# Kernel tuning notes

Measured on AMD Instinct MI355X. Metric: run time of the kernel, lower is better.

Reference implementation:

```python
import jax, jax.numpy as jnp
import numpy as np

N, E, IN_DIM, HID, L = 50000, 800000, 64, 64, 3
EDGE_DIM = 2 * HID + 2  # src_h | dst_h | edge_feat


def setup_inputs() -> dict:
    key = jax.random.key(0)
    ks = jax.random.split(key, 32)
    s = 0.05
    inp = {
        "h": jax.random.normal(ks[0], (N, IN_DIM), jnp.float32),
        "e": jax.random.normal(ks[1], (E, 2), jnp.float32),
        "src": jax.random.randint(ks[2], (E,), 0, N),
        "dst": jax.random.randint(ks[3], (E,), 0, N),
        # input embedding
        "emb_W": jax.random.normal(ks[4], (IN_DIM, HID), jnp.float32) * s,
        "emb_b": jnp.zeros((HID,), jnp.float32),
        # per-GIN-layer params (stacked over L)
        "eps": jnp.zeros((L,), jnp.float32),  # learn_eps init 0
        "mlp_W1": jax.random.normal(ks[5], (L, HID, HID), jnp.float32) * s,
        "mlp_b1": jnp.zeros((L, HID), jnp.float32),
        "mlp_bn_s": jnp.ones((L, HID), jnp.float32),   # eval-mode BN folded: x*s+sh
        "mlp_bn_sh": jnp.zeros((L, HID), jnp.float32),
        "mlp_W2": jax.random.normal(ks[6], (L, HID, HID), jnp.float32) * s,
        "mlp_b2": jnp.zeros((L, HID), jnp.float32),
        "apply_bn_s": jnp.ones((L, HID), jnp.float32),
        "apply_bn_sh": jnp.zeros((L, HID), jnp.float32),
        "gin_bn_s": jnp.ones((L, HID), jnp.float32),
        "gin_bn_sh": jnp.zeros((L, HID), jnp.float32),
        # prediction heads (L+1 of them)
        "pred_W1": jax.random.normal(ks[7], (L + 1, EDGE_DIM, HID), jnp.float32) * s,
        "pred_b1": jnp.zeros((L + 1, HID), jnp.float32),
        "pred_W2": jax.random.normal(ks[8], (L + 1, HID, 1), jnp.float32) * s,
        "pred_b2": jnp.zeros((L + 1, 1), jnp.float32),
    }
    return inp


def reference(h, e, src, dst, emb_W, emb_b, eps,
              mlp_W1, mlp_b1, mlp_bn_s, mlp_bn_sh, mlp_W2, mlp_b2,
              apply_bn_s, apply_bn_sh, gin_bn_s, gin_bn_sh,
              pred_W1, pred_b1, pred_W2, pred_b2):
    n = h.shape[0]
    bn = lambda x, sc, sh: x * sc + sh  # eval-mode batchnorm (folded scale/shift)

    h = h @ emb_W + emb_b  # [N, HID]

    def edge_feat(hh):
        # gather node features onto edges: [E, 2*HID+2]
        return jnp.concatenate([hh[src], hh[dst], e], axis=1)

    def pred(ef, i):
        z = jax.nn.relu(ef @ pred_W1[i] + pred_b1[i])
        return z @ pred_W2[i] + pred_b2[i]  # [E, 1]

    score = pred(edge_feat(h), 0)
    for i in range(L):
        h_in = h
        # GIN sum aggregation: copy src features, sum at dst
        neigh = jax.ops.segment_sum(h[src], dst, num_segments=n)
        x = (1.0 + eps[i]) * h + neigh
        # MLP: Linear -> BN -> ReLU -> Linear
        x = jax.nn.relu(bn(x @ mlp_W1[i] + mlp_b1[i], mlp_bn_s[i], mlp_bn_sh[i]))
        x = x @ mlp_W2[i] + mlp_b2[i]
        # ApplyNodeFunc: BN -> ReLU
        x = jax.nn.relu(bn(x, apply_bn_s[i], apply_bn_sh[i]))
        # GINLayer post: BN -> ReLU -> residual (dropout=0 in eval)
        x = jax.nn.relu(bn(x, gin_bn_s[i], gin_bn_sh[i]))
        h = h_in + x
        score = score + pred(edge_feat(h), i + 1)
    return jax.nn.relu(score)
```

## Files before the change

kernel.cpp:

```cpp
#include <hip/hip_runtime.h>

typedef unsigned short ushort_t;
typedef unsigned int uint_t;

static __device__ __forceinline__ ushort_t f2bf(float f) {
    uint_t u = __float_as_uint(f);
    uint_t r = (u + 0x7FFFu + ((u >> 16) & 1u)) >> 16;
    return (ushort_t)r;
}
static __device__ __forceinline__ float bf2f(ushort_t u) {
    return __uint_as_float(((uint_t)u) << 16);
}

static __device__ __forceinline__ float edge_p(
    ushort4 a, float4 brow, float ex, float ey,
    float4 wc0, float4 wc1, float4 w2v)
{
    float z0 = bf2f(a.x) + brow.x + ex*wc0.x + ey*wc1.x; z0 = fmaxf(z0, 0.f);
    float z1 = bf2f(a.y) + brow.y + ex*wc0.y + ey*wc1.y; z1 = fmaxf(z1, 0.f);
    float z2 = bf2f(a.z) + brow.z + ex*wc0.z + ey*wc1.z; z2 = fmaxf(z2, 0.f);
    float z3 = bf2f(a.w) + brow.w + ex*wc0.w + ey*wc1.w; z3 = fmaxf(z3, 0.f);
    return z0*w2v.x + z1*w2v.y + z2*w2v.z + z3*w2v.w;
}

#define RED16(p) { p += __shfl_xor(p,1); p += __shfl_xor(p,2); \
                   p += __shfl_xor(p,4); p += __shfl_xor(p,8); }

__global__ __launch_bounds__(256) void k_count(
    const int* __restrict__ dst, int* __restrict__ deg, int E)
{
    int e = blockIdx.x * 256 + threadIdx.x;
    if (e < E) atomicAdd(&deg[dst[e]], 1);
}

__global__ __launch_bounds__(1024) void k_scanA(
    const int* __restrict__ deg, int* __restrict__ partial,
    int* __restrict__ bsum, int N)
{
    __shared__ int wsum[16];
    int tid = threadIdx.x, lane = tid & 63, wid = tid >> 6;
    int idx = blockIdx.x * 1024 + tid;
    int v = (idx < N) ? deg[idx] : 0;
    int x = v;
#pragma unroll
    for (int o = 1; o < 64; o <<= 1) {
        int t = __shfl_up(x, o, 64);
        if (lane >= o) x += t;
    }
    if (lane == 63) wsum[wid] = x;
    __syncthreads();
    if (wid == 0) {
        int s = (lane < 16) ? wsum[lane] : 0;
#pragma unroll
        for (int o = 1; o < 16; o <<= 1) {
            int t = __shfl_up(s, o, 64);
            if (lane >= o) s += t;
        }
        if (lane < 16) wsum[lane] = s;
    }
    __syncthreads();
    int woff = (wid > 0) ? wsum[wid - 1] : 0;
    if (idx < N) partial[idx] = woff + x - v;
    if (tid == 0) bsum[blockIdx.x] = wsum[15];
}

__global__ __launch_bounds__(256) void k_scanB(
    int* __restrict__ bsum, int nb, int* __restrict__ totalp)
{
    __shared__ int s[256];
    int tid = threadIdx.x;
    int v = (tid < nb) ? bsum[tid] : 0;
    s[tid] = v;
    __syncthreads();
#pragma unroll
    for (int off = 1; off < 256; off <<= 1) {
        int t = (tid >= off) ? s[tid - off] : 0;
        __syncthreads();
        s[tid] += t;
        __syncthreads();
    }
    if (tid < nb) bsum[tid] = s[tid] - v;
    if (tid == 0) totalp[0] = s[255];
}

__global__ __launch_bounds__(256) void k_scanC(
    int* __restrict__ offsets, const int* __restrict__ bsum,
    int* __restrict__ cursor, int N)
{
    int idx = blockIdx.x * 256 + threadIdx.x;
    if (idx >= N) return;
    int o = offsets[idx] + bsum[idx >> 10];
    offsets[idx] = o;
    cursor[idx] = o;
}

__global__ __launch_bounds__(256) void k_fill(
    const int* __restrict__ src, const int* __restrict__ dst,
    const float* __restrict__ ep, int* __restrict__ cursor,
    int4* __restrict__ entries, int E)
{
    int ei = blockIdx.x * 256 + threadIdx.x;
    if (ei >= E) return;
    int pos = atomicAdd(&cursor[dst[ei]], 1);
    float2 ev = *(const float2*)(ep + 2 * (size_t)ei);
    entries[pos] = make_int4(src[ei], ei, __float_as_int(ev.x), __float_as_int(ev.y));
}

__global__ __launch_bounds__(256) void k_embed_ab(
    const float* __restrict__ in, const float* __restrict__ W,
    const float* __restrict__ bias, float* __restrict__ hout,
    ushort_t* __restrict__ hbfout,
    const float* __restrict__ WA, const float* __restrict__ bA,
    const float* __restrict__ WB,
    ushort_t* __restrict__ A, ushort_t* __restrict__ B, int N)
{
    __shared__ float xs[16][68];
    const int row16 = threadIdx.x >> 4;
    const int li    = threadIdx.x & 15;
    const int r     = blockIdx.x * 16 + row16;
    if (r >= N) return;
    float4 x4 = *(const float4*)(in + (size_t)r * 64 + 4 * li);
    xs[row16][4*li+0] = x4.x; xs[row16][4*li+1] = x4.y;
    xs[row16][4*li+2] = x4.z; xs[row16][4*li+3] = x4.w;
    float4 acc = *(const float4*)(bias + 4 * li);
#pragma unroll
    for (int k = 0; k < 64; k++) {
        float xk = xs[row16][k];
        float4 wv = *(const float4*)(W + k * 64 + 4 * li);
        acc.x += xk * wv.x; acc.y += xk * wv.y;
        acc.z += xk * wv.z; acc.w += xk * wv.w;
    }
    *(float4*)(hout + (size_t)r * 64 + 4 * li) = acc;
    if (hbfout) {
        ushort4 o;
        o.x = f2bf(acc.x); o.y = f2bf(acc.y); o.z = f2bf(acc.z); o.w = f2bf(acc.w);
        *(ushort4*)(hbfout + (size_t)r * 64 + 4 * li) = o;
    }
    xs[row16][4*li+0] = acc.x; xs[row16][4*li+1] = acc.y;
    xs[row16][4*li+2] = acc.z; xs[row16][4*li+3] = acc.w;
    float4 aA = *(const float4*)(bA + 4 * li);
    float4 aB = make_float4(0.f, 0.f, 0.f, 0.f);
#pragma unroll
    for (int k = 0; k < 64; k++) {
        float xk = xs[row16][k];
        float4 wa = *(const float4*)(WA + k * 64 + 4 * li);
        float4 wb = *(const float4*)(WB + k * 64 + 4 * li);
        aA.x += xk * wa.x; aA.y += xk * wa.y; aA.z += xk * wa.z; aA.w += xk * wa.w;
        aB.x += xk * wb.x; aB.y += xk * wb.y; aB.z += xk * wb.z; aB.w += xk * wb.w;
    }
    ushort4 oa, ob;
    oa.x = f2bf(aA.x); oa.y = f2bf(aA.y); oa.z = f2bf(aA.z); oa.w = f2bf(aA.w);
    ob.x = f2bf(aB.x); ob.y = f2bf(aB.y); ob.z = f2bf(aB.z); ob.w = f2bf(aB.w);
    *(ushort4*)(A + (size_t)r * 64 + 4 * li) = oa;
    *(ushort4*)(B + (size_t)r * 64 + 4 * li) = ob;
}

__global__ __launch_bounds__(256) void k_matmulAB(
    const float* __restrict__ h, const float* __restrict__ WA,
    const float* __restrict__ bA, const float* __restrict__ WB,
    ushort_t* __restrict__ A, ushort_t* __restrict__ B, int N)
{
    __shared__ float xs[16][68];
    const int row16 = threadIdx.x >> 4;
    const int li    = threadIdx.x & 15;
    const int r     = blockIdx.x * 16 + row16;
    if (r >= N) return;
    float4 x4 = *(const float4*)(h + (size_t)r * 64 + 4 * li);
    xs[row16][4*li+0] = x4.x; xs[row16][4*li+1] = x4.y;
    xs[row16][4*li+2] = x4.z; xs[row16][4*li+3] = x4.w;
    float4 accA = *(const float4*)(bA + 4 * li);
    float4 accB = make_float4(0.f, 0.f, 0.f, 0.f);
#pragma unroll
    for (int k = 0; k < 64; k++) {
        float xk = xs[row16][k];
        float4 wa = *(const float4*)(WA + k * 64 + 4 * li);
        float4 wb = *(const float4*)(WB + k * 64 + 4 * li);
        accA.x += xk * wa.x; accA.y += xk * wa.y;
        accA.z += xk * wa.z; accA.w += xk * wa.w;
        accB.x += xk * wb.x; accB.y += xk * wb.y;
        accB.z += xk * wb.z; accB.w += xk * wb.w;
    }
    ushort4 oa, ob;
    oa.x = f2bf(accA.x); oa.y = f2bf(accA.y); oa.z = f2bf(accA.z); oa.w = f2bf(accA.w);
    ob.x = f2bf(accB.x); ob.y = f2bf(accB.y); ob.z = f2bf(accB.z); ob.w = f2bf(accB.w);
    *(ushort4*)(A + (size_t)r * 64 + 4 * li) = oa;
    *(ushort4*)(B + (size_t)r * 64 + 4 * li) = ob;
}

template <int MODE, int HASGIN, int AGGBF, int EPI>
__global__ __launch_bounds__(256) void k_fused(
    const float* __restrict__ h, float* __restrict__ hout,
    const ushort_t* __restrict__ hbf, ushort_t* __restrict__ hbfout,
    const ushort_t* __restrict__ A, const ushort_t* __restrict__ Bm,
    const int4* __restrict__ entries, const int* __restrict__ offsets,
    float* __restrict__ score_csr, float* __restrict__ score_out,
    const float* __restrict__ Wc, const float* __restrict__ W2v,
    const float* __restrict__ b2p, const float* __restrict__ epsp,
    const float* __restrict__ W1, const float* __restrict__ b1,
    const float* __restrict__ s1, const float* __restrict__ sh1,
    const float* __restrict__ W2, const float* __restrict__ b2,
    const float* __restrict__ as_, const float* __restrict__ ash,
    const float* __restrict__ gs, const float* __restrict__ gsh,
    const float* __restrict__ WAn, const float* __restrict__ bAn,
    const float* __restrict__ WBn,
    ushort_t* __restrict__ Aout, ushort_t* __restrict__ Bout, int N)
{
    __shared__ float xs[16][68];
    __shared__ float ts[16][68];
    const int row16 = threadIdx.x >> 4;
    const int li    = threadIdx.x & 15;
    const int r     = blockIdx.x * 16 + row16;
    if (r >= N) return;

    const float4 wc0 = *(const float4*)(Wc + li*4);
    const float4 wc1 = *(const float4*)(Wc + 64 + li*4);
    const float4 w2v = *(const float4*)(W2v + li*4);
    const float bb2 = b2p[0];
    ushort4 bu = *(const ushort4*)(Bm + (size_t)r * 64 + li*4);
    const float4 brow = make_float4(bf2f(bu.x), bf2f(bu.y), bf2f(bu.z), bf2f(bu.w));

    const int beg = offsets[r], end = offsets[r + 1];
    float4 acc = make_float4(0.f, 0.f, 0.f, 0.f);

    int k = beg;
    for (; k + 3 < end; k += 4) {
        int4 e0 = entries[k], e1 = entries[k+1], e2 = entries[k+2], e3 = entries[k+3];
        ushort4 a0 = *(const ushort4*)(A + (size_t)e0.x * 64 + li*4);
        ushort4 a1 = *(const ushort4*)(A + (size_t)e1.x * 64 + li*4);
        ushort4 a2 = *(const ushort4*)(A + (size_t)e2.x * 64 + li*4);
        ushort4 a3 = *(const ushort4*)(A + (size_t)e3.x * 64 + li*4);
        if (HASGIN) {
            if (AGGBF) {
                ushort4 g0 = *(const ushort4*)(hbf + (size_t)e0.x * 64 + li*4);
                ushort4 g1 = *(const ushort4*)(hbf + (size_t)e1.x * 64 + li*4);
                ushort4 g2 = *(const ushort4*)(hbf + (size_t)e2.x * 64 + li*4);
                ushort4 g3 = *(const ushort4*)(hbf + (size_t)e3.x * 64 + li*4);
                acc.x += bf2f(g0.x) + bf2f(g1.x) + bf2f(g2.x) + bf2f(g3.x);
                acc.y += bf2f(g0.y) + bf2f(g1.y) + bf2f(g2.y) + bf2f(g3.y);
                acc.z += bf2f(g0.z) + bf2f(g1.z) + bf2f(g2.z) + bf2f(g3.z);
                acc.w += bf2f(g0.w) + bf2f(g1.w) + bf2f(g2.w) + bf2f(g3.w);
            } else {
                float4 g0 = *(const float4*)(h + (size_t)e0.x * 64 + li*4);
                float4 g1 = *(const float4*)(h + (size_t)e1.x * 64 + li*4);
                float4 g2 = *(const float4*)(h + (size_t)e2.x * 64 + li*4);
                float4 g3 = *(const float4*)(h + (size_t)e3.x * 64 + li*4);
                acc.x += g0.x + g1.x + g2.x + g3.x;
                acc.y += g0.y + g1.y + g2.y + g3.y;
                acc.z += g0.z + g1.z + g2.z + g3.z;
                acc.w += g0.w + g1.w + g2.w + g3.w;
            }
        }
        float p0 = edge_p(a0, brow, __int_as_float(e0.z), __int_as_float(e0.w), wc0, wc1, w2v);
        float p1 = edge_p(a1, brow, __int_as_float(e1.z), __int_as_float(e1.w), wc0, wc1, w2v);
        float p2 = edge_p(a2, brow, __int_as_float(e2.z), __int_as_float(e2.w), wc0, wc1, w2v);
        float p3 = edge_p(a3, brow, __int_as_float(e3.z), __int_as_float(e3.w), wc0, wc1, w2v);
        RED16(p0) RED16(p1) RED16(p2) RED16(p3)
        if (li == 0) {
            if (MODE == 0) {
                score_csr[k]   = p0 + bb2; score_csr[k+1] = p1 + bb2;
                score_csr[k+2] = p2 + bb2; score_csr[k+3] = p3 + bb2;
            } else if (MODE == 1) {
                score_csr[k]   += p0 + bb2; score_csr[k+1] += p1 + bb2;
                score_csr[k+2] += p2 + bb2; score_csr[k+3] += p3 + bb2;
            } else {
                score_out[e0.y] = fmaxf(score_csr[k]   + p0 + bb2, 0.f);
                score_out[e1.y] = fmaxf(score_csr[k+1] + p1 + bb2, 0.f);
                score_out[e2.y] = fmaxf(score_csr[k+2] + p2 + bb2, 0.f);
                score_out[e3.y] = fmaxf(score_csr[k+3] + p3 + bb2, 0.f);
            }
        }
    }
    for (; k < end; k++) {
        int4 e0 = entries[k];
        ushort4 a0 = *(const ushort4*)(A + (size_t)e0.x * 64 + li*4);
        if (HASGIN) {
            if (AGGBF) {
                ushort4 g0 = *(const ushort4*)(hbf + (size_t)e0.x * 64 + li*4);
                acc.x += bf2f(g0.x); acc.y += bf2f(g0.y);
                acc.z += bf2f(g0.z); acc.w += bf2f(g0.w);
            } else {
                float4 g0 = *(const float4*)(h + (size_t)e0.x * 64 + li*4);
                acc.x += g0.x; acc.y += g0.y; acc.z += g0.z; acc.w += g0.w;
            }
        }
        float p0 = edge_p(a0, brow, __int_as_float(e0.z), __int_as_float(e0.w), wc0, wc1, w2v);
        RED16(p0)
        if (li == 0) {
            if (MODE == 0)      score_csr[k] = p0 + bb2;
            else if (MODE == 1) score_csr[k] += p0 + bb2;
            else score_out[e0.y] = fmaxf(score_csr[k] + p0 + bb2, 0.f);
        }
    }

    if (!HASGIN) return;

    const float epsv = 1.0f + epsp[0];
    float4 hv = *(const float4*)(h + (size_t)r * 64 + 4 * li);
    xs[row16][4*li+0] = epsv * hv.x + acc.x;
    xs[row16][4*li+1] = epsv * hv.y + acc.y;
    xs[row16][4*li+2] = epsv * hv.z + acc.z;
    xs[row16][4*li+3] = epsv * hv.w + acc.w;

    float4 t = *(const float4*)(b1 + 4 * li);
#pragma unroll
    for (int kk = 0; kk < 64; kk++) {
        float xk = xs[row16][kk];
        float4 wv = *(const float4*)(W1 + kk * 64 + 4 * li);
        t.x += xk * wv.x; t.y += xk * wv.y; t.z += xk * wv.z; t.w += xk * wv.w;
    }
    {
        float4 sc = *(const float4*)(s1 + 4 * li);
        float4 sh = *(const float4*)(sh1 + 4 * li);
        t.x = fmaxf(t.x * sc.x + sh.x, 0.f);
        t.y = fmaxf(t.y * sc.y + sh.y, 0.f);
        t.z = fmaxf(t.z * sc.z + sh.z, 0.f);
        t.w = fmaxf(t.w * sc.w + sh.w, 0.f);
    }
    ts[row16][4*li+0] = t.x; ts[row16][4*li+1] = t.y;
    ts[row16][4*li+2] = t.z; ts[row16][4*li+3] = t.w;

    float4 u = *(const float4*)(b2 + 4 * li);
#pragma unroll
    for (int kk = 0; kk < 64; kk++) {
        float tk = ts[row16][kk];
        float4 wv = *(const float4*)(W2 + kk * 64 + 4 * li);
        u.x += tk * wv.x; u.y += tk * wv.y; u.z += tk * wv.z; u.w += tk * wv.w;
    }
    {
        float4 sc = *(const float4*)(as_ + 4 * li);
        float4 sh = *(const float4*)(ash + 4 * li);
        u.x = fmaxf(u.x * sc.x + sh.x, 0.f);
        u.y = fmaxf(u.y * sc.y + sh.y, 0.f);
        u.z = fmaxf(u.z * sc.z + sh.z, 0.f);
        u.w = fmaxf(u.w * sc.w + sh.w, 0.f);
        sc = *(const float4*)(gs + 4 * li);
        sh = *(const float4*)(gsh + 4 * li);
        u.x = fmaxf(u.x * sc.x + sh.x, 0.f);
        u.y = fmaxf(u.y * sc.y + sh.y, 0.f);
        u.z = fmaxf(u.z * sc.z + sh.z, 0.f);
        u.w = fmaxf(u.w * sc.w + sh.w, 0.f);
    }
    float4 o = make_float4(hv.x + u.x, hv.y + u.y, hv.z + u.z, hv.w + u.w);
    *(float4*)(hout + (size_t)r * 64 + 4 * li) = o;
    if (AGGBF) {
        ushort4 ob;
        ob.x = f2bf(o.x); ob.y = f2bf(o.y); ob.z = f2bf(o.z); ob.w = f2bf(o.w);
        *(ushort4*)(hbfout + (size_t)r * 64 + 4 * li) = ob;
    }

    if (EPI) {
        xs[row16][4*li+0] = o.x; xs[row16][4*li+1] = o.y;
        xs[row16][4*li+2] = o.z; xs[row16][4*li+3] = o.w;
        float4 aA = *(const float4*)(bAn + 4 * li);
        float4 aB = make_float4(0.f, 0.f, 0.f, 0.f);
#pragma unroll
        for (int kk = 0; kk < 64; kk++) {
            float xk = xs[row16][kk];
            float4 wa = *(const float4*)(WAn + kk * 64 + 4 * li);
            float4 wb = *(const float4*)(WBn + kk * 64 + 4 * li);
            aA.x += xk * wa.x; aA.y += xk * wa.y; aA.z += xk * wa.z; aA.w += xk * wa.w;
            aB.x += xk * wb.x; aB.y += xk * wb.y; aB.z += xk * wb.z; aB.w += xk * wb.w;
        }
        ushort4 oa, ob;
        oa.x = f2bf(aA.x); oa.y = f2bf(aA.y); oa.z = f2bf(aA.z); oa.w = f2bf(aA.w);
        ob.x = f2bf(aB.x); ob.y = f2bf(aB.y); ob.z = f2bf(aB.z); ob.w = f2bf(aB.w);
        *(ushort4*)(Aout + (size_t)r * 64 + li*4) = oa;
        *(ushort4*)(Bout + (size_t)r * 64 + li*4) = ob;
    }
}

extern "C" void kernel_launch(void* const* d_in, const int* in_sizes, int n_in,
                              void* d_out, int out_size, void* d_ws, size_t ws_size,
                              hipStream_t stream) {
    const float* h_in  = (const float*)d_in[0];
    const float* e     = (const float*)d_in[1];
    const int*   src   = (const int*)d_in[2];
    const int*   dst   = (const int*)d_in[3];
    const float* emb_W = (const float*)d_in[4];
    const float* emb_b = (const float*)d_in[5];
    const float* eps   = (const float*)d_in[6];
    const float* mW1   = (const float*)d_in[7];
    const float* mb1   = (const float*)d_in[8];
    const float* mbs   = (const float*)d_in[9];
    const float* mbsh  = (const float*)d_in[10];
    const float* mW2   = (const float*)d_in[11];
    const float* mb2   = (const float*)d_in[12];
    const float* as_   = (const float*)d_in[13];
    const float* ash   = (const float*)d_in[14];
    const float* gs    = (const float*)d_in[15];
    const float* gsh   = (const float*)d_in[16];
    const float* pW1   = (const float*)d_in[17];
    const float* pb1   = (const float*)d_in[18];
    const float* pW2   = (const float*)d_in[19];
    const float* pb2   = (const float*)d_in[20];

    const int N  = in_sizes[0] / 64;
    const int E  = in_sizes[2];
    const int Lr = in_sizes[6];
    const size_t nrow = (size_t)N * 64;

    float* score = (float*)d_out;

    char* wp = (char*)d_ws;
    auto take = [&](size_t b) -> char* {
        char* p = wp; wp += (b + 255) & ~(size_t)255; return p;
    };
    float*    h0        = (float*)take(nrow * 4);
    float*    h1        = (float*)take(nrow * 4);
    ushort_t* A0        = (ushort_t*)take(nrow * 2);
    ushort_t* B0        = (ushort_t*)take(nrow * 2);
    int4*     entries   = (int4*)take((size_t)E * 16);
    float*    score_csr = (float*)take((size_t)E * 4);
    int*      offsets   = (int*)take((size_t)(N + 1) * 4);
    int*      cursor    = (int*)take((size_t)N * 4);
    int*      bsum      = (int*)take(1024);
    ushort_t* hbf0      = (ushort_t*)take(nrow * 2);
    ushort_t* hbf1      = (ushort_t*)take(nrow * 2);
    size_t need_bf = (size_t)(wp - (char*)d_ws);
    ushort_t* A1        = (ushort_t*)take(nrow * 2);
    ushort_t* B1        = (ushort_t*)take(nrow * 2);
    size_t need_epi = (size_t)(wp - (char*)d_ws);

    const bool use_bf  = ws_size >= need_bf;
    const bool use_epi = ws_size >= need_epi;
    if (!use_bf) { hbf0 = nullptr; hbf1 = nullptr; }

    const int rowBlocks = (N + 15) / 16;
    const int edgeGrid  = (E + 255) / 256;
    const int nb        = (N + 1023) / 1024;

    hipMemsetAsync(cursor, 0, (size_t)N * sizeof(int), stream);
    k_count<<<edgeGrid, 256, 0, stream>>>(dst, cursor, E);
    k_scanA<<<nb, 1024, 0, stream>>>(cursor, offsets, bsum, N);
    k_scanB<<<1, 256, 0, stream>>>(bsum, nb, offsets + N);
    k_scanC<<<(N + 255) / 256, 256, 0, stream>>>(offsets, bsum, cursor, N);
    k_fill<<<edgeGrid, 256, 0, stream>>>(src, dst, e, cursor, entries, E);

    k_embed_ab<<<rowBlocks, 256, 0, stream>>>(
        h_in, emb_W, emb_b, h0, hbf0, pW1, pb1, pW1 + 64 * 64, A0, B0, N);

    float* hcur = h0;      float* hnext = h1;
    ushort_t* bcur = hbf0; ushort_t* bnext = hbf1;
    ushort_t* Acur = A0;   ushort_t* Bcur = B0;
    ushort_t* Aalt = use_epi ? A1 : A0;
    ushort_t* Balt = use_epi ? B1 : B0;

    for (int i = 0; i < Lr; i++) {
        const float* pw  = pW1 + (size_t)i * 130 * 64;
        const float* Wc  = pw + 128 * 64;
        const float* w2  = pW2 + (size_t)i * 64;
        const float* b2  = pb2 + i;
        const float* pwn = pW1 + (size_t)(i + 1) * 130 * 64;
        const float* gW1 = mW1 + (size_t)i * 64 * 64;
        const float* gW2 = mW2 + (size_t)i * 64 * 64;

        if (use_epi) {
            if (i == 0)
                k_fused<0,1,1,1><<<rowBlocks, 256, 0, stream>>>(
                    hcur, hnext, bcur, bnext, Acur, Bcur, entries, offsets,
                    score_csr, nullptr, Wc, w2, b2, eps + i,
                    gW1, mb1 + i*64, mbs + i*64, mbsh + i*64, gW2, mb2 + i*64,
                    as_ + i*64, ash + i*64, gs + i*64, gsh + i*64,
                    pwn, pb1 + (i+1)*64, pwn + 64*64, Aalt, Balt, N);
            else
                k_fused<1,1,1,1><<<rowBlocks, 256, 0, stream>>>(
                    hcur, hnext, bcur, bnext, Acur, Bcur, entries, offsets,
                    score_csr, nullptr, Wc, w2, b2, eps + i,
                    gW1, mb1 + i*64, mbs + i*64, mbsh + i*64, gW2, mb2 + i*64,
                    as_ + i*64, ash + i*64, gs + i*64, gsh + i*64,
                    pwn, pb1 + (i+1)*64, pwn + 64*64, Aalt, Balt, N);
            { ushort_t* t = Acur; Acur = Aalt; Aalt = t; }
            { ushort_t* t = Bcur; Bcur = Balt; Balt = t; }
        } else if (use_bf) {
            if (i == 0)
                k_fused<0,1,1,0><<<rowBlocks, 256, 0, stream>>>(
                    hcur, hnext, bcur, bnext, Acur, Bcur, entries, offsets,
                    score_csr, nullptr, Wc, w2, b2, eps + i,
                    gW1, mb1 + i*64, mbs + i*64, mbsh + i*64, gW2, mb2 + i*64,
                    as_ + i*64, ash + i*64, gs + i*64, gsh + i*64,
                    nullptr, nullptr, nullptr, nullptr, nullptr, N);
            else
                k_fused<1,1,1,0><<<rowBlocks, 256, 0, stream>>>(
                    hcur, hnext, bcur, bnext, Acur, Bcur, entries, offsets,
                    score_csr, nullptr, Wc, w2, b2, eps + i,
                    gW1, mb1 + i*64, mbs + i*64, mbsh + i*64, gW2, mb2 + i*64,
                    as_ + i*64, ash + i*64, gs + i*64, gsh + i*64,
                    nullptr, nullptr, nullptr, nullptr, nullptr, N);
            k_matmulAB<<<rowBlocks, 256, 0, stream>>>(
                hnext, pwn, pb1 + (i+1)*64, pwn + 64*64, A0, B0, N);
        } else {
            if (i == 0)
                k_fused<0,1,0,0><<<rowBlocks, 256, 0, stream>>>(
                    hcur, hnext, bcur, bnext, Acur, Bcur, entries, offsets,
                    score_csr, nullptr, Wc, w2, b2, eps + i,
                    gW1, mb1 + i*64, mbs + i*64, mbsh + i*64, gW2, mb2 + i*64,
                    as_ + i*64, ash + i*64, gs + i*64, gsh + i*64,
                    nullptr, nullptr, nullptr, nullptr, nullptr, N);
            else
                k_fused<1,1,0,0><<<rowBlocks, 256, 0, stream>>>(
                    hcur, hnext, bcur, bnext, Acur, Bcur, entries, offsets,
                    score_csr, nullptr, Wc, w2, b2, eps + i,
                    gW1, mb1 + i*64, mbs + i*64, mbsh + i*64, gW2, mb2 + i*64,
                    as_ + i*64, ash + i*64, gs + i*64, gsh + i*64,
                    nullptr, nullptr, nullptr, nullptr, nullptr, N);
            k_matmulAB<<<rowBlocks, 256, 0, stream>>>(
                hnext, pwn, pb1 + (i+1)*64, pwn + 64*64, A0, B0, N);
        }
        { float* t = hcur; hcur = hnext; hnext = t; }
        { ushort_t* t = bcur; bcur = bnext; bnext = t; }
    }

    {
        const float* pw = pW1 + (size_t)Lr * 130 * 64;
        const float* Wc = pw + 128 * 64;
        const float* w2 = pW2 + (size_t)Lr * 64;
        const float* b2 = pb2 + Lr;
        k_fused<2,0,0,0><<<rowBlocks, 256, 0, stream>>>(
            hcur, nullptr, nullptr, nullptr, Acur, Bcur, entries, offsets,
            score_csr, score, Wc, w2, b2, nullptr,
            nullptr, nullptr, nullptr, nullptr, nullptr, nullptr,
            nullptr, nullptr, nullptr, nullptr,
            nullptr, nullptr, nullptr, nullptr, nullptr, N);
    }
}
```

Baseline: 616.4 us.

## Interleave A-table and bf16 h into one gather row; process nodes in degree-sorted order

Stores the per-node prediction table A and the bf16 copy of h interleaved in a single 128-element row. Each neighbour gather then fetches one contiguous 16-byte chunk per lane instead of two separate 8-byte loads from different arrays. It also adds a bucket sort of nodes by in-degree and makes the fused kernel walk nodes through that permutation, so rows with similar edge counts share a block and load is better balanced. This costs three small preprocessing kernels plus an extra indirection per row, and removes the non-bf16 fallback path.

```diff
diff --git a/kernel.cpp b/kernel.cpp
--- a/kernel.cpp
+++ b/kernel.cpp
@@ -11,15 +11,24 @@
 static __device__ __forceinline__ float bf2f(ushort_t u) {
     return __uint_as_float(((uint_t)u) << 16);
 }
-
-static __device__ __forceinline__ float edge_p(
-    ushort4 a, float4 brow, float ex, float ey,
+static __device__ __forceinline__ float bf2f_lo(uint_t u) {
+    return __uint_as_float(u << 16);
+}
+static __device__ __forceinline__ float bf2f_hi(uint_t u) {
+    return __uint_as_float(u & 0xffff0000u);
+}
+static __device__ __forceinline__ uint_t pack2(float lo, float hi) {
+    return (uint_t)f2bf(lo) | ((uint_t)f2bf(hi) << 16);
+}
+
+static __device__ __forceinline__ float edge_p2(
+    uint_t ax, uint_t ay, float4 brow, float ex, float ey,
     float4 wc0, float4 wc1, float4 w2v)
 {
-    float z0 = bf2f(a.x) + brow.x + ex*wc0.x + ey*wc1.x; z0 = fmaxf(z0, 0.f);
-    float z1 = bf2f(a.y) + brow.y + ex*wc0.y + ey*wc1.y; z1 = fmaxf(z1, 0.f);
-    float z2 = bf2f(a.z) + brow.z + ex*wc0.z + ey*wc1.z; z2 = fmaxf(z2, 0.f);
-    float z3 = bf2f(a.w) + brow.w + ex*wc0.w + ey*wc1.w; z3 = fmaxf(z3, 0.f);
+    float z0 = bf2f_lo(ax) + brow.x + ex*wc0.x + ey*wc1.x; z0 = fmaxf(z0, 0.f);
+    float z1 = bf2f_hi(ax) + brow.y + ex*wc0.y + ey*wc1.y; z1 = fmaxf(z1, 0.f);
+    float z2 = bf2f_lo(ay) + brow.z + ex*wc0.z + ey*wc1.z; z2 = fmaxf(z2, 0.f);
+    float z3 = bf2f_hi(ay) + brow.w + ex*wc0.w + ey*wc1.w; z3 = fmaxf(z3, 0.f);
     return z0*w2v.x + z1*w2v.y + z2*w2v.z + z3*w2v.w;
 }
 
@@ -106,13 +115,79 @@
     entries[pos] = make_int4(src[ei], ei, __float_as_int(ev.x), __float_as_int(ev.y));
 }
 
+static __device__ __forceinline__ int deg_bucket(int d) {
+    return d >= 63 ? 0 : (63 - d);
+}
+
+__global__ __launch_bounds__(256) void k_bcount(
+    const int* __restrict__ offsets, int* __restrict__ bcnt, int N)
+{
+    int idx = blockIdx.x * 256 + threadIdx.x;
+    if (idx >= N) return;
+    int d = offsets[idx + 1] - offsets[idx];
+    atomicAdd(&bcnt[deg_bucket(d)], 1);
+}
+
+__global__ __launch_bounds__(64) void k_bscan(
+    int* __restrict__ bcnt, int* __restrict__ bcur)
+{
+    int lane = threadIdx.x;
+    int v = bcnt[lane];
+    int x = v;
+#pragma unroll
+    for (int o = 1; o < 64; o <<= 1) {
+        int t = __shfl_up(x, o, 64);
+        if (lane >= o) x += t;
+    }
+    bcur[lane] = x - v;
+}
+
+__global__ __launch_bounds__(256) void k_bfill(
+    const int* __restrict__ offsets, int* __restrict__ bcur,
+    int* __restrict__ perm, int N)
+{
+    int idx = blockIdx.x * 256 + threadIdx.x;
+    if (idx >= N) return;
+    int d = offsets[idx + 1] - offsets[idx];
+    int pos = atomicAdd(&bcur[deg_bucket(d)], 1);
+    perm[pos] = idx;
+}
+
+static __device__ __forceinline__ void epi_tables16(
+    float (*xs)[68], int row16, int li, int r, float4 o,
+    const float* __restrict__ WAn, const float* __restrict__ bAn,
+    const float* __restrict__ WBn,
+    ushort_t* __restrict__ comb_out, ushort_t* __restrict__ B_out)
+{
+    xs[row16][4*li+0] = o.x; xs[row16][4*li+1] = o.y;
+    xs[row16][4*li+2] = o.z; xs[row16][4*li+3] = o.w;
+    float4 aA = *(const float4*)(bAn + 4 * li);
+    float4 aB = make_float4(0.f, 0.f, 0.f, 0.f);
+#pragma unroll
+    for (int k = 0; k < 64; k++) {
+        float xk = xs[row16][k];
+        float4 wa = *(const float4*)(WAn + k * 64 + 4 * li);
+        float4 wb = *(const float4*)(WBn + k * 64 + 4 * li);
+        aA.x += xk * wa.x; aA.y += xk * wa.y; aA.z += xk * wa.z; aA.w += xk * wa.w;
+        aB.x += xk * wb.x; aB.y += xk * wb.y; aB.z += xk * wb.z; aB.w += xk * wb.w;
+    }
+    int4 cw;
+    cw.x = (int)pack2(aA.x, aA.y);
+    cw.y = (int)pack2(aA.z, aA.w);
+    cw.z = (int)pack2(o.x, o.y);
+    cw.w = (int)pack2(o.z, o.w);
+    *(int4*)(comb_out + (size_t)r * 128 + li * 8) = cw;
+    ushort4 ob;
+    ob.x = f2bf(aB.x); ob.y = f2bf(aB.y); ob.z = f2bf(aB.z); ob.w = f2bf(aB.w);
+    *(ushort4*)(B_out + (size_t)r * 64 + 4 * li) = ob;
+}
+
 __global__ __launch_bounds__(256) void k_embed_ab(
     const float* __restrict__ in, const float* __restrict__ W,
     const float* __restrict__ bias, float* __restrict__ hout,
-    ushort_t* __restrict__ hbfout,
     const float* __restrict__ WA, const float* __restrict__ bA,
     const float* __restrict__ WB,
-    ushort_t* __restrict__ A, ushort_t* __restrict__ B, int N)
+    ushort_t* __restrict__ comb_out, ushort_t* __restrict__ B_out, int N)
 {
     __shared__ float xs[16][68];
     const int row16 = threadIdx.x >> 4;
@@ -131,68 +206,30 @@
         acc.z += xk * wv.z; acc.w += xk * wv.w;
     }
     *(float4*)(hout + (size_t)r * 64 + 4 * li) = acc;
-    if (hbfout) {
-        ushort4 o;
-        o.x = f2bf(acc.x); o.y = f2bf(acc.y); o.z = f2bf(acc.z); o.w = f2bf(acc.w);
-        *(ushort4*)(hbfout + (size_t)r * 64 + 4 * li) = o;
-    }
-    xs[row16][4*li+0] = acc.x; xs[row16][4*li+1] = acc.y;
-    xs[row16][4*li+2] = acc.z; xs[row16][4*li+3] = acc.w;
-    float4 aA = *(const float4*)(bA + 4 * li);
-    float4 aB = make_float4(0.f, 0.f, 0.f, 0.f);
-#pragma unroll
-    for (int k = 0; k < 64; k++) {
-        float xk = xs[row16][k];
-        float4 wa = *(const float4*)(WA + k * 64 + 4 * li);
-        float4 wb = *(const float4*)(WB + k * 64 + 4 * li);
-        aA.x += xk * wa.x; aA.y += xk * wa.y; aA.z += xk * wa.z; aA.w += xk * wa.w;
-        aB.x += xk * wb.x; aB.y += xk * wb.y; aB.z += xk * wb.z; aB.w += xk * wb.w;
-    }
-    ushort4 oa, ob;
-    oa.x = f2bf(aA.x); oa.y = f2bf(aA.y); oa.z = f2bf(aA.z); oa.w = f2bf(aA.w);
-    ob.x = f2bf(aB.x); ob.y = f2bf(aB.y); ob.z = f2bf(aB.z); ob.w = f2bf(aB.w);
-    *(ushort4*)(A + (size_t)r * 64 + 4 * li) = oa;
-    *(ushort4*)(B + (size_t)r * 64 + 4 * li) = ob;
-}
-
-__global__ __launch_bounds__(256) void k_matmulAB(
-    const float* __restrict__ h, const float* __restrict__ WA,
-    const float* __restrict__ bA, const float* __restrict__ WB,
-    ushort_t* __restrict__ A, ushort_t* __restrict__ B, int N)
+    epi_tables16(xs, row16, li, r, acc, WA, bA, WB, comb_out, B_out);
+}
+
+__global__ __launch_bounds__(256) void k_tables(
+    const float* __restrict__ h,
+    const float* __restrict__ WA, const float* __restrict__ bA,
+    const float* __restrict__ WB,
+    ushort_t* __restrict__ comb_out, ushort_t* __restrict__ B_out, int N)
 {
     __shared__ float xs[16][68];
     const int row16 = threadIdx.x >> 4;
     const int li    = threadIdx.x & 15;
     const int r     = blockIdx.x * 16 + row16;
     if (r >= N) return;
-    float4 x4 = *(const float4*)(h + (size_t)r * 64 + 4 * li);
-    xs[row16][4*li+0] = x4.x; xs[row16][4*li+1] = x4.y;
-    xs[row16][4*li+2] = x4.z; xs[row16][4*li+3] = x4.w;
-    float4 accA = *(const float4*)(bA + 4 * li);
-    float4 accB = make_float4(0.f, 0.f, 0.f, 0.f);
-#pragma unroll
-    for (int k = 0; k < 64; k++) {
-        float xk = xs[row16][k];
-        float4 wa = *(const float4*)(WA + k * 64 + 4 * li);
-        float4 wb = *(const float4*)(WB + k * 64 + 4 * li);
-        accA.x += xk * wa.x; accA.y += xk * wa.y;
-        accA.z += xk * wa.z; accA.w += xk * wa.w;
-        accB.x += xk * wb.x; accB.y += xk * wb.y;
-        accB.z += xk * wb.z; accB.w += xk * wb.w;
-    }
-    ushort4 oa, ob;
-    oa.x = f2bf(accA.x); oa.y = f2bf(accA.y); oa.z = f2bf(accA.z); oa.w = f2bf(accA.w);
-    ob.x = f2bf(accB.x); ob.y = f2bf(accB.y); ob.z = f2bf(accB.z); ob.w = f2bf(accB.w);
-    *(ushort4*)(A + (size_t)r * 64 + 4 * li) = oa;
-    *(ushort4*)(B + (size_t)r * 64 + 4 * li) = ob;
-}
-
-template <int MODE, int HASGIN, int AGGBF, int EPI>
+    float4 o = *(const float4*)(h + (size_t)r * 64 + 4 * li);
+    epi_tables16(xs, row16, li, r, o, WA, bA, WB, comb_out, B_out);
+}
+
+template <int MODE, int HASGIN, int EPI>
 __global__ __launch_bounds__(256) void k_fused(
     const float* __restrict__ h, float* __restrict__ hout,
-    const ushort_t* __restrict__ hbf, ushort_t* __restrict__ hbfout,
-    const ushort_t* __restrict__ A, const ushort_t* __restrict__ Bm,
+    const ushort_t* __restrict__ comb, const ushort_t* __restrict__ Bm,
     const int4* __restrict__ entries, const int* __restrict__ offsets,
+    const int* __restrict__ perm,
     float* __restrict__ score_csr, float* __restrict__ score_out,
     const float* __restrict__ Wc, const float* __restrict__ W2v,
     const float* __restrict__ b2p, const float* __restrict__ epsp,
@@ -203,14 +240,15 @@
     const float* __restrict__ gs, const float* __restrict__ gsh,
     const float* __restrict__ WAn, const float* __restrict__ bAn,
     const float* __restrict__ WBn,
-    ushort_t* __restrict__ Aout, ushort_t* __restrict__ Bout, int N)
+    ushort_t* __restrict__ comb_out, ushort_t* __restrict__ B_out, int N)
 {
     __shared__ float xs[16][68];
     __shared__ float ts[16][68];
     const int row16 = threadIdx.x >> 4;
     const int li    = threadIdx.x & 15;
-    const int r     = blockIdx.x * 16 + row16;
-    if (r >= N) return;
+    const int idx   = blockIdx.x * 16 + row16;
+    if (idx >= N) return;
+    const int r = perm[idx];
 
     const float4 wc0 = *(const float4*)(Wc + li*4);
     const float4 wc1 = *(const float4*)(Wc + 64 + li*4);
@@ -225,35 +263,34 @@
     int k = beg;
     for (; k + 3 < end; k += 4) {
         int4 e0 = entries[k], e1 = entries[k+1], e2 = entries[k+2], e3 = entries[k+3];
-        ushort4 a0 = *(const ushort4*)(A + (size_t)e0.x * 64 + li*4);
-        ushort4 a1 = *(const ushort4*)(A + (size_t)e1.x * 64 + li*4);
-        ushort4 a2 = *(const ushort4*)(A + (size_t)e2.x * 64 + li*4);
-        ushort4 a3 = *(const ushort4*)(A + (size_t)e3.x * 64 + li*4);
+        uint_t ax0, ay0, ax1, ay1, ax2, ay2, ax3, ay3;
         if (HASGIN) {
-            if (AGGBF) {
-                ushort4 g0 = *(const ushort4*)(hbf + (size_t)e0.x * 64 + li*4);
-                ushort4 g1 = *(const ushort4*)(hbf + (size_t)e1.x * 64 + li*4);
-                ushort4 g2 = *(const ushort4*)(hbf + (size_t)e2.x * 64 + li*4);
-                ushort4 g3 = *(const ushort4*)(hbf + (size_t)e3.x * 64 + li*4);
-                acc.x += bf2f(g0.x) + bf2f(g1.x) + bf2f(g2.x) + bf2f(g3.x);
-                acc.y += bf2f(g0.y) + bf2f(g1.y) + bf2f(g2.y) + bf2f(g3.y);
-                acc.z += bf2f(g0.z) + bf2f(g1.z) + bf2f(g2.z) + bf2f(g3.z);
-                acc.w += bf2f(g0.w) + bf2f(g1.w) + bf2f(g2.w) + bf2f(g3.w);
-            } else {
-                float4 g0 = *(const float4*)(h + (size_t)e0.x * 64 + li*4);
-                float4 g1 = *(const float4*)(h + (size_t)e1.x * 64 + li*4);
-                float4 g2 = *(const float4*)(h + (size_t)e2.x * 64 + li*4);
-                float4 g3 = *(const float4*)(h + (size_t)e3.x * 64 + li*4);
-                acc.x += g0.x + g1.x + g2.x + g3.x;
-                acc.y += g0.y + g1.y + g2.y + g3.y;
-                acc.z += g0.z + g1.z + g2.z + g3.z;
-                acc.w += g0.w + g1.w + g2.w + g3.w;
-            }
+            int4 c0 = *(const int4*)(comb + (size_t)e0.x * 128 + li * 8);
+            int4 c1 = *(const int4*)(comb + (size_t)e1.x * 128 + li * 8);
+            int4 c2 = *(const int4*)(comb + (size_t)e2.x * 128 + li * 8);
+            int4 c3 = *(const int4*)(comb + (size_t)e3.x * 128 + li * 8);
+            acc.x += bf2f_lo(c0.z) + bf2f_lo(c1.z) + bf2f_lo(c2.z) + bf2f_lo(c3.z);
+            acc.y += bf2f_hi(c0.z) + bf2f_hi(c1.z) + bf2f_hi(c2.z) + bf2f_hi(c3.z);
+            acc.z += bf2f_lo(c0.w) + bf2f_lo(c1.w) + bf2f_lo(c2.w) + bf2f_lo(c3.w);
+            acc.w += bf2f_hi(c0.w) + bf2f_hi(c1.w) + bf2f_hi(c2.w) + bf2f_hi(c3.w);
+            ax0 = (uint_t)c0.x; ay0 = (uint_t)c0.y;
+            ax1 = (uint_t)c1.x; ay1 = (uint_t)c1.y;
+            ax2 = (uint_t)c2.x; ay2 = (uint_t)c2.y;
+            ax3 = (uint_t)c3.x; ay3 = (uint_t)c3.y;
+        } else {
+            int2 d0 = *(const int2*)(comb + (size_t)e0.x * 128 + li * 8);
+            int2 d1 = *(const int2*)(comb + (size_t)e1.x * 128 + li * 8);
+            int2 d2 = *(const int2*)(comb + (size_t)e2.x * 128 + li * 8);
+            int2 d3 = *(const int2*)(comb + (size_t)e3.x * 128 + li * 8);
+            ax0 = (uint_t)d0.x; ay0 = (uint_t)d0.y;
+            ax1 = (uint_t)d1.x; ay1 = (uint_t)d1.y;
+            ax2 = (uint_t)d2.x; ay2 = (uint_t)d2.y;
+            ax3 = (uint_t)d3.x; ay3 = (uint_t)d3.y;
         }
-        float p0 = edge_p(a0, brow, __int_as_float(e0.z), __int_as_float(e0.w), wc0, wc1, w2v);
-        float p1 = edge_p(a1, brow, __int_as_float(e1.z), __int_as_float(e1.w), wc0, wc1, w2v);
-        float p2 = edge_p(a2, brow, __int_as_float(e2.z), __int_as_float(e2.w), wc0, wc1, w2v);
-        float p3 = edge_p(a3, brow, __int_as_float(e3.z), __int_as_float(e3.w), wc0, wc1, w2v);
+        float p0 = edge_p2(ax0, ay0, brow, __int_as_float(e0.z), __int_as_float(e0.w), wc0, wc1, w2v);
+        float p1 = edge_p2(ax1, ay1, brow, __int_as_float(e1.z), __int_as_float(e1.w), wc0, wc1, w2v);
+        float p2 = edge_p2(ax2, ay2, brow, __int_as_float(e2.z), __int_as_float(e2.w), wc0, wc1, w2v);
+        float p3 = edge_p2(ax3, ay3, brow, __int_as_float(e3.z), __int_as_float(e3.w), wc0, wc1, w2v);
         RED16(p0) RED16(p1) RED16(p2) RED16(p3)
         if (li == 0) {
             if (MODE == 0) {
@@ -272,18 +309,17 @@
     }
     for (; k < end; k++) {
         int4 e0 = entries[k];
-        ushort4 a0 = *(const ushort4*)(A + (size_t)e0.x * 64 + li*4);
+        uint_t ax0, ay0;
         if (HASGIN) {
-            if (AGGBF) {
-                ushort4 g0 = *(const ushort4*)(hbf + (size_t)e0.x * 64 + li*4);
-                acc.x += bf2f(g0.x); acc.y += bf2f(g0.y);
-                acc.z += bf2f(g0.z); acc.w += bf2f(g0.w);
-            } else {
-                float4 g0 = *(const float4*)(h + (size_t)e0.x * 64 + li*4);
-                acc.x += g0.x; acc.y += g0.y; acc.z += g0.z; acc.w += g0.w;
-            }
+            int4 c0 = *(const int4*)(comb + (size_t)e0.x * 128 + li * 8);
+            acc.x += bf2f_lo(c0.z); acc.y += bf2f_hi(c0.z);
+            acc.z += bf2f_lo(c0.w); acc.w += bf2f_hi(c0.w);
+            ax0 = (uint_t)c0.x; ay0 = (uint_t)c0.y;
+        } else {
+            int2 d0 = *(const int2*)(comb + (size_t)e0.x * 128 + li * 8);
+            ax0 = (uint_t)d0.x; ay0 = (uint_t)d0.y;
         }
-        float p0 = edge_p(a0, brow, __int_as_float(e0.z), __int_as_float(e0.w), wc0, wc1, w2v);
+        float p0 = edge_p2(ax0, ay0, brow, __int_as_float(e0.z), __int_as_float(e0.w), wc0, wc1, w2v);
         RED16(p0)
         if (li == 0) {
             if (MODE == 0)      score_csr[k] = p0 + bb2;
@@ -342,31 +378,9 @@
     }
     float4 o = make_float4(hv.x + u.x, hv.y + u.y, hv.z + u.z, hv.w + u.w);
     *(float4*)(hout + (size_t)r * 64 + 4 * li) = o;
-    if (AGGBF) {
-        ushort4 ob;
-        ob.x = f2bf(o.x); ob.y = f2bf(o.y); ob.z = f2bf(o.z); ob.w = f2bf(o.w);
-        *(ushort4*)(hbfout + (size_t)r * 64 + 4 * li) = ob;
-    }
-
-    if (EPI) {
-        xs[row16][4*li+0] = o.x; xs[row16][4*li+1] = o.y;
-        xs[row16][4*li+2] = o.z; xs[row16][4*li+3] = o.w;
-        float4 aA = *(const float4*)(bAn + 4 * li);
-        float4 aB = make_float4(0.f, 0.f, 0.f, 0.f);
-#pragma unroll
-        for (int kk = 0; kk < 64; kk++) {
-            float xk = xs[row16][kk];
-            float4 wa = *(const float4*)(WAn + kk * 64 + 4 * li);
-            float4 wb = *(const float4*)(WBn + kk * 64 + 4 * li);
-            aA.x += xk * wa.x; aA.y += xk * wa.y; aA.z += xk * wa.z; aA.w += xk * wa.w;
-            aB.x += xk * wb.x; aB.y += xk * wb.y; aB.z += xk * wb.z; aB.w += xk * wb.w;
-        }
-        ushort4 oa, ob;
-        oa.x = f2bf(aA.x); oa.y = f2bf(aA.y); oa.z = f2bf(aA.z); oa.w = f2bf(aA.w);
-        ob.x = f2bf(aB.x); ob.y = f2bf(aB.y); ob.z = f2bf(aB.z); ob.w = f2bf(aB.w);
-        *(ushort4*)(Aout + (size_t)r * 64 + li*4) = oa;
-        *(ushort4*)(Bout + (size_t)r * 64 + li*4) = ob;
-    }
+
+    if (EPI)
+        epi_tables16(xs, row16, li, r, o, WAn, bAn, WBn, comb_out, B_out);
 }
 
 extern "C" void kernel_launch(void* const* d_in, const int* in_sizes, int n_in,
@@ -407,23 +421,21 @@
     };
     float*    h0        = (float*)take(nrow * 4);
     float*    h1        = (float*)take(nrow * 4);
-    ushort_t* A0        = (ushort_t*)take(nrow * 2);
+    ushort_t* comb0     = (ushort_t*)take(nrow * 4);
     ushort_t* B0        = (ushort_t*)take(nrow * 2);
     int4*     entries   = (int4*)take((size_t)E * 16);
     float*    score_csr = (float*)take((size_t)E * 4);
     int*      offsets   = (int*)take((size_t)(N + 1) * 4);
     int*      cursor    = (int*)take((size_t)N * 4);
     int*      bsum      = (int*)take(1024);
-    ushort_t* hbf0      = (ushort_t*)take(nrow * 2);
-    ushort_t* hbf1      = (ushort_t*)take(nrow * 2);
-    size_t need_bf = (size_t)(wp - (char*)d_ws);
-    ushort_t* A1        = (ushort_t*)take(nrow * 2);
+    int*      perm      = (int*)take((size_t)N * 4);
+    int*      bcnt      = (int*)take(64 * 4);
+    int*      bcur      = (int*)take(64 * 4);
+    ushort_t* comb1     = (ushort_t*)take(nrow * 4);
     ushort_t* B1        = (ushort_t*)take(nrow * 2);
     size_t need_epi = (size_t)(wp - (char*)d_ws);
 
-    const bool use_bf  = ws_size >= need_bf;
     const bool use_epi = ws_size >= need_epi;
-    if (!use_bf) { hbf0 = nullptr; hbf1 = nullptr; }
 
     const int rowBlocks = (N + 15) / 16;
     const int edgeGrid  = (E + 255) / 256;
@@ -436,14 +448,17 @@
     k_scanC<<<(N + 255) / 256, 256, 0, stream>>>(offsets, bsum, cursor, N);
     k_fill<<<edgeGrid, 256, 0, stream>>>(src, dst, e, cursor, entries, E);
 
+    hipMemsetAsync(bcnt, 0, 64 * sizeof(int), stream);
+    k_bcount<<<(N + 255) / 256, 256, 0, stream>>>(offsets, bcnt, N);
+    k_bscan<<<1, 64, 0, stream>>>(bcnt, bcur);
+    k_bfill<<<(N + 255) / 256, 256, 0, stream>>>(offsets, bcur, perm, N);
+
     k_embed_ab<<<rowBlocks, 256, 0, stream>>>(
-        h_in, emb_W, emb_b, h0, hbf0, pW1, pb1, pW1 + 64 * 64, A0, B0, N);
-
-    float* hcur = h0;      float* hnext = h1;
-    ushort_t* bcur = hbf0; ushort_t* bnext = hbf1;
-    ushort_t* Acur = A0;   ushort_t* Bcur = B0;
-    ushort_t* Aalt = use_epi ? A1 : A0;
-    ushort_t* Balt = use_epi ? B1 : B0;
+        h_in, emb_W, emb_b, h0, pW1, pb1, pW1 + 64 * 64, comb0, B0, N);
+
+    float* hcur = h0;       float* hnext = h1;
+    ushort_t* Ccur = comb0; ushort_t* Cnxt = use_epi ? comb1 : comb0;
+    ushort_t* Bcur = B0;    ushort_t* Bnxt = use_epi ? B1 : B0;
 
     for (int i = 0; i < Lr; i++) {
         const float* pw  = pW1 + (size_t)i * 130 * 64;
@@ -456,58 +471,40 @@
 
         if (use_epi) {
             if (i == 0)
-                k_fused<0,1,1,1><<<rowBlocks, 256, 0, stream>>>(
-                    hcur, hnext, bcur, bnext, Acur, Bcur, entries, offsets,
-                    score_csr, nullptr, Wc, w2, b2, eps + i,
+                k_fused<0,1,1><<<rowBlocks, 256, 0, stream>>>(
+                    hcur, hnext, Ccur, Bcur, entries, offsets, perm, score_csr, nullptr,
+                    Wc, w2, b2, eps + i,
                     gW1, mb1 + i*64, mbs + i*64, mbsh + i*64, gW2, mb2 + i*64,
                     as_ + i*64, ash + i*64, gs + i*64, gsh + i*64,
-                    pwn, pb1 + (i+1)*64, pwn + 64*64, Aalt, Balt, N);
+                    pwn, pb1 + (i+1)*64, pwn + 64*64, Cnxt, Bnxt, N);
             else
-                k_fused<1,1,1,1><<<rowBlocks, 256, 0, stream>>>(
-                    hcur, hnext, bcur, bnext, Acur, Bcur, entries, offsets,
-                    score_csr, nullptr, Wc, w2, b2, eps + i,
+                k_fused<1,1,1><<<rowBlocks, 256, 0, stream>>>(
+                    hcur, hnext, Ccur, Bcur, entries, offsets, perm, score_csr, nullptr,
+                    Wc, w2, b2, eps + i,
                     gW1, mb1 + i*64, mbs + i*64, mbsh + i*64, gW2, mb2 + i*64,
                     as_ + i*64, ash + i*64, gs + i*64, gsh + i*64,
-                    pwn, pb1 + (i+1)*64, pwn + 64*64, Aalt, Balt, N);
-            { ushort_t* t = Acur; Acur = Aalt; Aalt = t; }
-            { ushort_t* t = Bcur; Bcur = Balt; Balt = t; }
-        } else if (use_bf) {
+                    pwn, pb1 + (i+1)*64, pwn + 64*64, Cnxt, Bnxt, N);
+            { ushort_t* t = Ccur; Ccur = Cnxt; Cnxt = t; }
+            { ushort_t* t = Bcur; Bcur = Bnxt; Bnxt = t; }
+        } else {
             if (i == 0)
-                k_fused<0,1,1,0><<<rowBlocks, 256, 0, stream>>>(
-                    hcur, hnext, bcur, bnext, Acur, Bcur, entries, offsets,
-                    score_csr, nullptr, Wc, w2, b2, eps + i,
+                k_fused<0,1,0><<<rowBlocks, 256, 0, stream>>>(
+                    hcur, hnext, Ccur, Bcur, entries, offsets, perm, score_csr, nullptr,
+                    Wc, w2, b2, eps + i,
                     gW1, mb1 + i*64, mbs + i*64, mbsh + i*64, gW2, mb2 + i*64,
                     as_ + i*64, ash + i*64, gs + i*64, gsh + i*64,
                     nullptr, nullptr, nullptr, nullptr, nullptr, N);
             else
-                k_fused<1,1,1,0><<<rowBlocks, 256, 0, stream>>>(
-                    hcur, hnext, bcur, bnext, Acur, Bcur, entries, offsets,
-                    score_csr, nullptr, Wc, w2, b2, eps + i,
+                k_fused<1,1,0><<<rowBlocks, 256, 0, stream>>>(
+                    hcur, hnext, Ccur, Bcur, entries, offsets, perm, score_csr, nullptr,
+                    Wc, w2, b2, eps + i,
                     gW1, mb1 + i*64, mbs + i*64, mbsh + i*64, gW2, mb2 + i*64,
                     as_ + i*64, ash + i*64, gs + i*64, gsh + i*64,
                     nullptr, nullptr, nullptr, nullptr, nullptr, N);
-            k_matmulAB<<<rowBlocks, 256, 0, stream>>>(
-                hnext, pwn, pb1 + (i+1)*64, pwn + 64*64, A0, B0, N);
-        } else {
-            if (i == 0)
-                k_fused<0,1,0,0><<<rowBlocks, 256, 0, stream>>>(
-                    hcur, hnext, bcur, bnext, Acur, Bcur, entries, offsets,
-                    score_csr, nullptr, Wc, w2, b2, eps + i,
-                    gW1, mb1 + i*64, mbs + i*64, mbsh + i*64, gW2, mb2 + i*64,
-                    as_ + i*64, ash + i*64, gs + i*64, gsh + i*64,
-                    nullptr, nullptr, nullptr, nullptr, nullptr, N);
-            else
-                k_fused<1,1,0,0><<<rowBlocks, 256, 0, stream>>>(
-                    hcur, hnext, bcur, bnext, Acur, Bcur, entries, offsets,
-                    score_csr, nullptr, Wc, w2, b2, eps + i,
-                    gW1, mb1 + i*64, mbs + i*64, mbsh + i*64, gW2, mb2 + i*64,
-                    as_ + i*64, ash + i*64, gs + i*64, gsh + i*64,
-                    nullptr, nullptr, nullptr, nullptr, nullptr, N);
-            k_matmulAB<<<rowBlocks, 256, 0, stream>>>(
-                hnext, pwn, pb1 + (i+1)*64, pwn + 64*64, A0, B0, N);
+            k_tables<<<rowBlocks, 256, 0, stream>>>(
+                hnext, pwn, pb1 + (i+1)*64, pwn + 64*64, Ccur, Bcur, N);
         }
         { float* t = hcur; hcur = hnext; hnext = t; }
-        { ushort_t* t = bcur; bcur = bnext; bnext = t; }
     }
 
     {
@@ -515,9 +512,9 @@
         const float* Wc = pw + 128 * 64;
         const float* w2 = pW2 + (size_t)Lr * 64;
         const float* b2 = pb2 + Lr;
-        k_fused<2,0,0,0><<<rowBlocks, 256, 0, stream>>>(
-            hcur, nullptr, nullptr, nullptr, Acur, Bcur, entries, offsets,
-            score_csr, score, Wc, w2, b2, nullptr,
+        k_fused<2,0,0><<<rowBlocks, 256, 0, stream>>>(
+            hcur, nullptr, Ccur, Bcur, entries, offsets, perm, score_csr, score,
+            Wc, w2, b2, nullptr,
             nullptr, nullptr, nullptr, nullptr, nullptr, nullptr,
             nullptr, nullptr, nullptr, nullptr,
             nullptr, nullptr, nullptr, nullptr, nullptr, N);
```

Result: slower. 855.8 us (+38.8%).
